# Kernel optimization log

Hardware: AMD Instinct MI355X
Metric: run time of the kernel (lower is better)

The kernel has to match this reference:

```python
import jax, jax.numpy as jnp
import numpy as np

EPS = 1.1920929e-07  # torch RMSNorm default eps = float32 finfo eps

def rms_norm(x, w):
    return x * jax.lax.rsqrt(jnp.mean(x * x, axis=-1, keepdims=True) + EPS) * w

def setup_inputs() -> dict:
    key = jax.random.key(0)
    ks = jax.random.split(key, 10)
    B, C, H, W = 8, 64, 48, 48
    E = C  # embed_dim = query_dim = key_dim = value_dim
    q = jax.random.normal(ks[0], (B, C, H, W), jnp.float32)
    k = jax.random.normal(ks[1], (B, C, H, W), jnp.float32)
    v = jax.random.normal(ks[2], (B, C, H, W), jnp.float32)
    s = 1.0 / np.sqrt(E)
    conv_w = jax.random.normal(ks[3], (C, C, 3, 3), jnp.float32) * (1.0 / np.sqrt(C * 9))
    nq_w = jnp.ones((E,), jnp.float32)
    nk_w = jnp.ones((E,), jnp.float32)
    wq = jax.random.normal(ks[4], (E, E), jnp.float32) * s
    bq = jax.random.normal(ks[5], (E,), jnp.float32) * 0.01
    wk = jax.random.normal(ks[6], (E, E), jnp.float32) * s
    bk = jax.random.normal(ks[7], (E,), jnp.float32) * 0.01
    return {"q": q, "k": k, "v": v, "conv_w": conv_w, "nq_w": nq_w,
            "nk_w": nk_w, "wq": wq, "bq": bq, "wk": wk, "bk": bk}

def reference(q, k, v, conv_w, nq_w, nk_w, wq, bq, wk, bk):
    B, C, H, W = q.shape
    num_heads = 4
    head_dim = C // num_heads
    # conv2d 3x3, stride 1, same padding, no bias
    qc = jax.lax.conv_general_dilated(
        q, conv_w, window_strides=(1, 1), padding='SAME',
        dimension_numbers=('NCHW', 'OIHW', 'NCHW'))
    # b c h w -> b (h w) c
    qs = qc.reshape(B, C, H * W).transpose(0, 2, 1)
    ksq = k.reshape(B, C, -1).transpose(0, 2, 1)
    vsq = v.reshape(B, C, -1).transpose(0, 2, 1)
    # RMSNorm on q and k (norm_v output feeds MHA value path whose output is discarded)
    qn = rms_norm(qs, nq_w)
    kn = rms_norm(ksq, nk_w)
    # MHA projections (q scaled by 1/sqrt(head_dim) as in torch)
    qp = (qn @ wq.T + bq) * (1.0 / np.sqrt(head_dim))
    kp = ksq_p = kn @ wk.T + bk
    Sq, Sk = qp.shape[1], kp.shape[1]
    qh = qp.reshape(B, Sq, num_heads, head_dim)
    kh = kp.reshape(B, Sk, num_heads, head_dim)
    scores = jnp.einsum('bihd,bjhd->bhij', qh, kh)
    attn = jax.nn.softmax(scores, axis=-1)
    # average_attn_weights=True -> mean over heads
    attn_avg = jnp.mean(attn, axis=1)  # [b, i, j]
    # custom output: weighted sum over RAW (un-normed, unprojected) value
    out = jnp.einsum('bij,bjd->bid', attn_avg, vsq)
    return out
```

## Files before the change

### kernel.cpp

```cpp
#include <hip/hip_runtime.h>
#include <hip/hip_bf16.h>

namespace {
constexpr int kB = 8;
constexpr int kC = 64;
constexpr int kH = 48;
constexpr int kW = 48;
constexpr int kS = kH * kW;
constexpr float kEps = 1.1920929e-07f;
constexpr float kQScale = 0.25f * 1.4426950408889634f;
}

typedef __attribute__((ext_vector_type(8))) short short8;
typedef __attribute__((ext_vector_type(4))) float f32x4;

__device__ __forceinline__ short f2bf(float x) {
  unsigned u = __float_as_uint(x);
  u += 0x7fffu + ((u >> 16) & 1u);
  return (short)(u >> 16);
}
__device__ __forceinline__ float bf2f(short s) {
  return __uint_as_float(((unsigned)(unsigned short)s) << 16);
}
__device__ __forceinline__ float fexp2(float x) {
  return __builtin_amdgcn_exp2f(x);
}

__global__ __launch_bounds__(256) void fused_prep(
    const float* __restrict__ q, const float* __restrict__ k,
    const float* __restrict__ v, const float* __restrict__ wq,
    const float* __restrict__ wk, const float* __restrict__ conv_w,
    short* __restrict__ qt, short* __restrict__ kt, short* __restrict__ vt,
    short* __restrict__ wqb3, short* __restrict__ wkb3, short* __restrict__ wt3) {
  const int blk = blockIdx.x;
  if (blk < 576) {
    __shared__ float tile[64][65];
    const int zz = blk / 36;
    const int bx = blk % 36;
    const int b = zz >> 1;
    const float* src = (zz & 1) ? k : q;
    short* dst = (zz & 1) ? kt : qt;
    const int s0 = bx * 64;
    const int tx = threadIdx.x & 63;
    const int ty = threadIdx.x >> 6;
#pragma unroll
    for (int r = 0; r < 16; ++r) {
      int c = r * 4 + ty;
      tile[c][tx] = src[((size_t)b * kC + c) * kS + s0 + tx];
    }
    __syncthreads();
#pragma unroll
    for (int r = 0; r < 16; ++r) {
      int s = r * 4 + ty;
      dst[((size_t)b * kS + s0 + s) * kC + tx] = f2bf(tile[tx][s]);
    }
  } else if (blk < 1728) {
    int idx = ((blk - 576) * 256 + threadIdx.x) * 4;
    float4 x = *reinterpret_cast<const float4*>(v + idx);
    int2 o;
    o.x = ((int)(unsigned short)f2bf(x.y) << 16) | (unsigned short)f2bf(x.x);
    o.y = ((int)(unsigned short)f2bf(x.w) << 16) | (unsigned short)f2bf(x.z);
    *reinterpret_cast<int2*>(vt + idx) = o;
  } else {
    int idx = (blk - 1728) * 256 + threadIdx.x;
    if (idx < 4096) {
      int j = idx & 7, Lw = (idx >> 3) & 63, slab = idx >> 9;
      int nt = slab & 3, kh = slab >> 2;
      int e = nt * 16 + (Lw & 15), c = kh * 32 + (Lw >> 4) * 8 + j;
      wqb3[idx] = f2bf(wq[e * 64 + c]);
    } else if (idx < 8192) {
      int i2 = idx - 4096;
      int j = i2 & 7, Lw = (i2 >> 3) & 63, slab = i2 >> 9;
      int nt = slab & 3, kh = slab >> 2;
      int e = nt * 16 + (Lw & 15), c = kh * 32 + (Lw >> 4) * 8 + j;
      wkb3[i2] = f2bf(wk[e * 64 + c]);
    } else {
      int i3 = idx - 8192;
      int j = i3 & 7, Lw = (i3 >> 3) & 63, slab = i3 >> 9;
      int nt = slab & 3, kh = (slab >> 2) & 1, tap = slab >> 3;
      int co = nt * 16 + (Lw & 15), ci = kh * 32 + (Lw >> 4) * 8 + j;
      wt3[i3] = f2bf(conv_w[co * 576 + ci * 9 + tap]);
    }
  }
}

__global__ __launch_bounds__(256) void fused_qk_gemm(
    const short* __restrict__ qt, const short* __restrict__ kt,
    const short* __restrict__ wt3, const short* __restrict__ wqb3,
    const short* __restrict__ wkb3,
    const float* __restrict__ nq_w, const float* __restrict__ nk_w,
    const float* __restrict__ bq, const float* __restrict__ bk,
    short* __restrict__ qp, short* __restrict__ kp) {
  __shared__ __align__(16) short Qs[164][72];
  __shared__ __align__(16) short ln[4][16][80];
  const int blk = blockIdx.x;
  const int t = threadIdx.x;
  const int ws = t >> 6;
  const int L = t & 63;
  const int quad = L >> 4;
  const int l16 = L & 15;
  const short8 zero8 = {0, 0, 0, 0, 0, 0, 0, 0};

  if (blk < 288) {
    const int b = blk / 36;
    const int S0 = (blk % 36) * 64;
    const int sBase = S0 + ws * 16;
    const int s = sBase + l16;
    const int h = s / kW, w = s % kW;

    const short* qtb = qt + (size_t)b * kS * kC;
#pragma unroll
    for (int it = 0; it < 6; ++it) {
      int idx = it * 256 + t;
      if (idx < 164 * 8) {
        int r = idx >> 3, sg = idx & 7;
        int srow = S0 - 49 + r;
        srow = srow < 0 ? 0 : (srow >= kS ? kS - 1 : srow);
        *reinterpret_cast<int4*>(&Qs[r][sg * 8]) =
            *reinterpret_cast<const int4*>(qtb + (size_t)srow * kC + sg * 8);
      }
    }
    __syncthreads();

    const int baseLocal = ws * 16 + l16 + 49;
    f32x4 acc[4] = {{0.f, 0.f, 0.f, 0.f}, {0.f, 0.f, 0.f, 0.f},
                    {0.f, 0.f, 0.f, 0.f}, {0.f, 0.f, 0.f, 0.f}};
#pragma unroll
    for (int tap = 0; tap < 9; ++tap) {
      const int dh = tap / 3 - 1, dw = tap % 3 - 1;
      const bool valid = (unsigned)(h + dh) < (unsigned)kH &&
                         (unsigned)(w + dw) < (unsigned)kW;
      const int local = baseLocal + dh * kW + dw;
#pragma unroll
      for (int kh = 0; kh < 2; ++kh) {
        short8 af = *reinterpret_cast<const short8*>(&Qs[local][kh * 32 + quad * 8]);
        af = valid ? af : zero8;
        const short* wb = wt3 + ((tap * 2 + kh) * 4) * 512 + L * 8;
#pragma unroll
        for (int nt = 0; nt < 4; ++nt) {
          short8 bf = *reinterpret_cast<const short8*>(wb + nt * 512);
          acc[nt] = __builtin_amdgcn_mfma_f32_16x16x32_bf16(af, bf, acc[nt], 0, 0, 0);
        }
      }
    }
    float rstd[4];
#pragma unroll
    for (int reg = 0; reg < 4; ++reg) {
      float pr = acc[0][reg] * acc[0][reg] + acc[1][reg] * acc[1][reg]
               + acc[2][reg] * acc[2][reg] + acc[3][reg] * acc[3][reg];
      pr += __shfl_xor(pr, 1, 64);
      pr += __shfl_xor(pr, 2, 64);
      pr += __shfl_xor(pr, 4, 64);
      pr += __shfl_xor(pr, 8, 64);
      rstd[reg] = rsqrtf(pr * (1.0f / kC) + kEps);
    }
#pragma unroll
    for (int nt = 0; nt < 4; ++nt) {
      float g = nq_w[nt * 16 + l16];
#pragma unroll
      for (int reg = 0; reg < 4; ++reg) {
        ln[ws][quad * 4 + reg][nt * 16 + l16] = f2bf(acc[nt][reg] * rstd[reg] * g);
      }
    }
    __syncthreads();
    f32x4 acc2[4] = {{0.f, 0.f, 0.f, 0.f}, {0.f, 0.f, 0.f, 0.f},
                     {0.f, 0.f, 0.f, 0.f}, {0.f, 0.f, 0.f, 0.f}};
#pragma unroll
    for (int kh = 0; kh < 2; ++kh) {
      short8 af = *reinterpret_cast<const short8*>(&ln[ws][l16][kh * 32 + quad * 8]);
      const short* wb = wqb3 + (kh * 4) * 512 + L * 8;
#pragma unroll
      for (int nt = 0; nt < 4; ++nt) {
        short8 bf = *reinterpret_cast<const short8*>(wb + nt * 512);
        acc2[nt] = __builtin_amdgcn_mfma_f32_16x16x32_bf16(af, bf, acc2[nt], 0, 0, 0);
      }
    }
#pragma unroll
    for (int nt = 0; nt < 4; ++nt) {
      const int e = nt * 16 + l16;
      float bias = bq[e];
#pragma unroll
      for (int reg = 0; reg < 4; ++reg) {
        qp[((size_t)b * kS + sBase + quad * 4 + reg) * kC + e] =
            f2bf((acc2[nt][reg] + bias) * kQScale);
      }
    }
  } else {
    const int idx = blk - 288;
    const int b = idx / 36;
    const int S0 = (idx % 36) * 64;
    const int sBase = S0 + ws * 16;

    const short* ktb = kt + ((size_t)b * kS + S0) * kC;
#pragma unroll
    for (int it = 0; it < 2; ++it) {
      int r = it * 32 + (t >> 3), sg = t & 7;
      *reinterpret_cast<int4*>(&Qs[r][sg * 8]) =
          *reinterpret_cast<const int4*>(ktb + (size_t)r * kC + sg * 8);
    }
    __syncthreads();

    short8 af0 = *reinterpret_cast<const short8*>(&Qs[ws * 16 + l16][quad * 8]);
    short8 af1 = *reinterpret_cast<const short8*>(&Qs[ws * 16 + l16][32 + quad * 8]);

    float xs[16];
#pragma unroll
    for (int j = 0; j < 8; ++j) { xs[j] = bf2f(af0[j]); xs[8 + j] = bf2f(af1[j]); }
    float sum = 0.f;
#pragma unroll
    for (int j = 0; j < 16; ++j) sum = fmaf(xs[j], xs[j], sum);
    sum += __shfl_xor(sum, 16, 64);
    sum += __shfl_xor(sum, 32, 64);
    float rstd = rsqrtf(sum * (1.0f / kC) + kEps);

    const float* n0 = nk_w + quad * 8;
#pragma unroll
    for (int j = 0; j < 8; ++j) {
      af0[j] = f2bf(xs[j] * rstd * n0[j]);
      af1[j] = f2bf(xs[8 + j] * rstd * n0[32 + j]);
    }

    f32x4 acc[4] = {{0.f, 0.f, 0.f, 0.f}, {0.f, 0.f, 0.f, 0.f},
                    {0.f, 0.f, 0.f, 0.f}, {0.f, 0.f, 0.f, 0.f}};
#pragma unroll
    for (int nt = 0; nt < 4; ++nt) {
      short8 bf0 = *reinterpret_cast<const short8*>(
          wkb3 + (0 * 4 + nt) * 512 + L * 8);
      short8 bf1 = *reinterpret_cast<const short8*>(
          wkb3 + (1 * 4 + nt) * 512 + L * 8);
      acc[nt] = __builtin_amdgcn_mfma_f32_16x16x32_bf16(af0, bf0, acc[nt], 0, 0, 0);
      acc[nt] = __builtin_amdgcn_mfma_f32_16x16x32_bf16(af1, bf1, acc[nt], 0, 0, 0);
    }
#pragma unroll
    for (int nt = 0; nt < 4; ++nt) {
      const int e = nt * 16 + l16;
      float bias = bk[e];
#pragma unroll
      for (int reg = 0; reg < 4; ++reg) {
        kp[((size_t)b * kS + sBase + quad * 4 + reg) * kC + e] =
            f2bf(acc[nt][reg] + bias);
      }
    }
  }
}

__global__ __launch_bounds__(256, 5) void attn_flash(
    const short* __restrict__ qp, const short* __restrict__ kp,
    const short* __restrict__ vt, float* __restrict__ out) {
  __shared__ __align__(16) short Kt[2][64][40];
  __shared__ __align__(16) short Vt[2][64][72];
  __shared__ float pl[4][16][2];
  __shared__ float Li[32][2];

  float* slabF = reinterpret_cast<float*>(&Kt[0][0][0]);

  const int blk = blockIdx.x;
  const int b = blk & 7;
  const int idx = blk >> 3;
  const int hp = idx & 1;
  const int i0 = (idx >> 1) * 32;
  const int t = threadIdx.x;
  const int ws = t >> 6;
  const int isub = ws & 1;
  const int jhalf = ws >> 1;
  const int jbase = jhalf * 32;
  const int L = t & 63;
  const int quad = L >> 4;
  const int l16 = L & 15;

  const f32x4 zc = {0.f, 0.f, 0.f, 0.f};
  const short8 z8 = {0, 0, 0, 0, 0, 0, 0, 0};

  const short* qrow = qp + ((size_t)b * kS + i0 + isub * 16 + l16) * kC + hp * 32;
  const short8 qw = *reinterpret_cast<const short8*>(qrow + quad * 8);
  const bool lo = quad < 2;
  const short8 qm[2] = {lo ? qw : z8, lo ? z8 : qw};

  const int rK = t >> 2;
  const int segK = t & 3;
  const int r8i = t >> 3;
  const int seg = t & 7;
  const short* kg = kp + (size_t)b * kS * kC + hp * 32;
  const short* vg = vt + (size_t)b * kC * kS;

  const int p32 = rK & 31;
  const int prowK =
      (rK & 32) | ((p32 & 4) << 2) | (((p32 >> 3) & 3) << 2) | (p32 & 3);

  int4 kreg, vreg[2];
  kreg = *reinterpret_cast<const int4*>(kg + (size_t)rK * kC + segK * 8);
#pragma unroll
  for (int pass = 0; pass < 2; ++pass)
    vreg[pass] = *reinterpret_cast<const int4*>(
        vg + (size_t)(pass * 32 + r8i) * kS + seg * 8);
  *reinterpret_cast<int4*>(&Kt[0][prowK][segK * 8]) = kreg;
#pragma unroll
  for (int pass = 0; pass < 2; ++pass)
    *reinterpret_cast<int4*>(&Vt[0][pass * 32 + r8i][seg * 8]) = vreg[pass];
  __syncthreads();

  f32x4 U[2][4];
#pragma unroll
  for (int hl = 0; hl < 2; ++hl)
#pragma unroll
    for (int d = 0; d < 4; ++d) U[hl][d] = zc;
  float lh[2] = {0.f, 0.f};

  for (int jt = 0; jt < kS / 64; ++jt) {
    const int buf = jt & 1;
    const bool more = (jt + 1) < kS / 64;
    if (more) {
      const int jn = (jt + 1) * 64;
      kreg = *reinterpret_cast<const int4*>(
          kg + (size_t)(jn + rK) * kC + segK * 8);
#pragma unroll
      for (int pass = 0; pass < 2; ++pass)
        vreg[pass] = *reinterpret_cast<const int4*>(
            vg + (size_t)(pass * 32 + r8i) * kS + jn + seg * 8);
    }

    short8 kf[2];
#pragma unroll
    for (int c = 0; c < 2; ++c)
      kf[c] = *reinterpret_cast<const short8*>(
          &Kt[buf][jbase + c * 16 + l16][quad * 8]);
    short8 vf[4];
#pragma unroll
    for (int d = 0; d < 4; ++d)
      vf[d] = *reinterpret_cast<const short8*>(
          &Vt[buf][d * 16 + l16][jbase + quad * 8]);

#pragma unroll
    for (int hl = 0; hl < 2; ++hl) {
      f32x4 s0 = __builtin_amdgcn_mfma_f32_16x16x32_bf16(kf[0], qm[hl], zc, 0, 0, 0);
      f32x4 s1 = __builtin_amdgcn_mfma_f32_16x16x32_bf16(kf[1], qm[hl], zc, 0, 0, 0);
      float e0 = fexp2(s0[0]), e1 = fexp2(s0[1]);
      float e2 = fexp2(s0[2]), e3 = fexp2(s0[3]);
      float f0 = fexp2(s1[0]), f1 = fexp2(s1[1]);
      float f2 = fexp2(s1[2]), f3 = fexp2(s1[3]);
      lh[hl] += ((e0 + e1) + (e2 + e3)) + ((f0 + f1) + (f2 + f3));
      union { __hip_bfloat162 h2[4]; short8 s8; } cv;
      cv.h2[0] = __float22bfloat162_rn(make_float2(e0, e1));
      cv.h2[1] = __float22bfloat162_rn(make_float2(e2, e3));
      cv.h2[2] = __float22bfloat162_rn(make_float2(f0, f1));
      cv.h2[3] = __float22bfloat162_rn(make_float2(f2, f3));
#pragma unroll
      for (int d = 0; d < 4; ++d)
        U[hl][d] = __builtin_amdgcn_mfma_f32_16x16x32_bf16(vf[d], cv.s8, U[hl][d], 0, 0, 0);
    }

    if (more) {
      const int nb = buf ^ 1;
      *reinterpret_cast<int4*>(&Kt[nb][prowK][segK * 8]) = kreg;
#pragma unroll
      for (int pass = 0; pass < 2; ++pass)
        *reinterpret_cast<int4*>(&Vt[nb][pass * 32 + r8i][seg * 8]) = vreg[pass];
    }
    __syncthreads();
  }

#pragma unroll
  for (int hl = 0; hl < 2; ++hl) {
    lh[hl] += __shfl_xor(lh[hl], 16, 64);
    lh[hl] += __shfl_xor(lh[hl], 32, 64);
  }
  if (quad == 0) {
#pragma unroll
    for (int hl = 0; hl < 2; ++hl) pl[ws][l16][hl] = lh[hl];
  }
  __syncthreads();
  if (t < 64) {
    const int i = t >> 1, h2 = t & 1;
    Li[i][h2] = 0.25f / (pl[i >> 4][i & 15][h2] + pl[(i >> 4) + 2][i & 15][h2]);
  }
  __syncthreads();
  float c2[2];
#pragma unroll
  for (int hl = 0; hl < 2; ++hl) c2[hl] = Li[isub * 16 + l16][hl];

#pragma unroll
  for (int d = 0; d < 4; ++d) {
    if (jhalf == 1) {
#pragma unroll
      for (int hl = 0; hl < 2; ++hl)
#pragma unroll
        for (int reg = 0; reg < 4; ++reg)
          slabF[((isub * 2 + hl) * 4 + reg) * 66 + L] = U[hl][d][reg];
    }
    __syncthreads();
    if (jhalf == 0) {
      float of[4] = {0.f, 0.f, 0.f, 0.f};
#pragma unroll
      for (int hl = 0; hl < 2; ++hl) {
#pragma unroll
        for (int reg = 0; reg < 4; ++reg) {
          float tot = U[hl][d][reg] + slabF[((isub * 2 + hl) * 4 + reg) * 66 + L];
          of[reg] += tot * c2[hl];
        }
      }
      float* op = out + ((size_t)b * kS + i0 + isub * 16 + l16) * kC + d * 16 + quad * 4;
#pragma unroll
      for (int reg = 0; reg < 4; ++reg) atomicAdd(op + reg, of[reg]);
    }
    __syncthreads();
  }
}

extern "C" void kernel_launch(void* const* d_in, const int* in_sizes, int n_in,
                              void* d_out, int out_size, void* d_ws, size_t ws_size,
                              hipStream_t stream) {
  const float* q      = (const float*)d_in[0];
  const float* k      = (const float*)d_in[1];
  const float* v      = (const float*)d_in[2];
  const float* conv_w = (const float*)d_in[3];
  const float* nq_w   = (const float*)d_in[4];
  const float* nk_w   = (const float*)d_in[5];
  const float* wq     = (const float*)d_in[6];
  const float* bq     = (const float*)d_in[7];
  const float* wk     = (const float*)d_in[8];
  const float* bk     = (const float*)d_in[9];
  float* out = (float*)d_out;

  const size_t N = (size_t)kB * kS * kC;
  short* qt   = (short*)d_ws;
  short* kt   = qt + N;
  short* vt   = kt + N;
  short* qp   = vt + N;
  short* kp   = qp + N;
  short* wqb3 = kp + N;
  short* wkb3 = wqb3 + 4096;
  short* wt3  = wkb3 + 4096;

  hipMemsetAsync(d_out, 0, out_size, stream);

  fused_prep<<<1904, 256, 0, stream>>>(q, k, v, wq, wk, conv_w,
                                       qt, kt, vt, wqb3, wkb3, wt3);
  fused_qk_gemm<<<576, 256, 0, stream>>>(qt, kt, wt3, wqb3, wkb3,
                                         nq_w, nk_w, bq, bk, qp, kp);
  attn_flash<<<1152, 256, 0, stream>>>(qp, kp, vt, out);
}
```

Measured before the change: 155.4 us.

## Load K/V fragments directly from global into registers, dropping LDS staging

```diff
diff --git a/kernel.cpp b/kernel.cpp
--- a/kernel.cpp
+++ b/kernel.cpp
@@ -244,15 +244,12 @@
   }
 }
 
-__global__ __launch_bounds__(256, 5) void attn_flash(
+__global__ __launch_bounds__(256, 4) void attn_flash(
     const short* __restrict__ qp, const short* __restrict__ kp,
     const short* __restrict__ vt, float* __restrict__ out) {
-  __shared__ __align__(16) short Kt[2][64][40];
-  __shared__ __align__(16) short Vt[2][64][72];
   __shared__ float pl[4][16][2];
   __shared__ float Li[32][2];
-
-  float* slabF = reinterpret_cast<float*>(&Kt[0][0][0]);
+  __shared__ __align__(16) float slab[16][66];
 
   const int blk = blockIdx.x;
   const int b = blk & 7;
@@ -263,7 +260,6 @@
   const int ws = t >> 6;
   const int isub = ws & 1;
   const int jhalf = ws >> 1;
-  const int jbase = jhalf * 32;
   const int L = t & 63;
   const int quad = L >> 4;
   const int l16 = L & 15;
@@ -276,28 +272,10 @@
   const bool lo = quad < 2;
   const short8 qm[2] = {lo ? qw : z8, lo ? z8 : qw};
 
-  const int rK = t >> 2;
-  const int segK = t & 3;
-  const int r8i = t >> 3;
-  const int seg = t & 7;
-  const short* kg = kp + (size_t)b * kS * kC + hp * 32;
-  const short* vg = vt + (size_t)b * kC * kS;
-
-  const int p32 = rK & 31;
-  const int prowK =
-      (rK & 32) | ((p32 & 4) << 2) | (((p32 >> 3) & 3) << 2) | (p32 & 3);
-
-  int4 kreg, vreg[2];
-  kreg = *reinterpret_cast<const int4*>(kg + (size_t)rK * kC + segK * 8);
-#pragma unroll
-  for (int pass = 0; pass < 2; ++pass)
-    vreg[pass] = *reinterpret_cast<const int4*>(
-        vg + (size_t)(pass * 32 + r8i) * kS + seg * 8);
-  *reinterpret_cast<int4*>(&Kt[0][prowK][segK * 8]) = kreg;
-#pragma unroll
-  for (int pass = 0; pass < 2; ++pass)
-    *reinterpret_cast<int4*>(&Vt[0][pass * 32 + r8i][seg * 8]) = vreg[pass];
-  __syncthreads();
+  const int permRow = ((l16 >> 2) << 3) | (l16 & 3);
+  const short* kbase =
+      kp + ((size_t)b * kS + jhalf * 32 + permRow) * kC + hp * 32 + quad * 8;
+  const short* vbase = vt + ((size_t)b * kC + l16) * kS + jhalf * 32 + quad * 8;
 
   f32x4 U[2][4];
 #pragma unroll
@@ -306,34 +284,33 @@
     for (int d = 0; d < 4; ++d) U[hl][d] = zc;
   float lh[2] = {0.f, 0.f};
 
+  short8 kn[2], vn[4];
+#pragma unroll
+  for (int c = 0; c < 2; ++c)
+    kn[c] = *reinterpret_cast<const short8*>(kbase + (size_t)c * 4 * kC);
+#pragma unroll
+  for (int d = 0; d < 4; ++d)
+    vn[d] = *reinterpret_cast<const short8*>(vbase + (size_t)d * 16 * kS);
+
   for (int jt = 0; jt < kS / 64; ++jt) {
-    const int buf = jt & 1;
-    const bool more = (jt + 1) < kS / 64;
-    if (more) {
-      const int jn = (jt + 1) * 64;
-      kreg = *reinterpret_cast<const int4*>(
-          kg + (size_t)(jn + rK) * kC + segK * 8);
-#pragma unroll
-      for (int pass = 0; pass < 2; ++pass)
-        vreg[pass] = *reinterpret_cast<const int4*>(
-            vg + (size_t)(pass * 32 + r8i) * kS + jn + seg * 8);
-    }
-
-    short8 kf[2];
-#pragma unroll
-    for (int c = 0; c < 2; ++c)
-      kf[c] = *reinterpret_cast<const short8*>(
-          &Kt[buf][jbase + c * 16 + l16][quad * 8]);
-    short8 vf[4];
-#pragma unroll
-    for (int d = 0; d < 4; ++d)
-      vf[d] = *reinterpret_cast<const short8*>(
-          &Vt[buf][d * 16 + l16][jbase + quad * 8]);
+    const short8 kf0 = kn[0], kf1 = kn[1];
+    const short8 vf0 = vn[0], vf1 = vn[1], vf2 = vn[2], vf3 = vn[3];
+
+    if (jt + 1 < kS / 64) {
+      const short* kb2 = kbase + (size_t)(jt + 1) * 64 * kC;
+      const short* vb2 = vbase + (size_t)(jt + 1) * 64;
+#pragma unroll
+      for (int c = 0; c < 2; ++c)
+        kn[c] = *reinterpret_cast<const short8*>(kb2 + (size_t)c * 4 * kC);
+#pragma unroll
+      for (int d = 0; d < 4; ++d)
+        vn[d] = *reinterpret_cast<const short8*>(vb2 + (size_t)d * 16 * kS);
+    }
 
 #pragma unroll
     for (int hl = 0; hl < 2; ++hl) {
-      f32x4 s0 = __builtin_amdgcn_mfma_f32_16x16x32_bf16(kf[0], qm[hl], zc, 0, 0, 0);
-      f32x4 s1 = __builtin_amdgcn_mfma_f32_16x16x32_bf16(kf[1], qm[hl], zc, 0, 0, 0);
+      f32x4 s0 = __builtin_amdgcn_mfma_f32_16x16x32_bf16(kf0, qm[hl], zc, 0, 0, 0);
+      f32x4 s1 = __builtin_amdgcn_mfma_f32_16x16x32_bf16(kf1, qm[hl], zc, 0, 0, 0);
       float e0 = fexp2(s0[0]), e1 = fexp2(s0[1]);
       float e2 = fexp2(s0[2]), e3 = fexp2(s0[3]);
       float f0 = fexp2(s1[0]), f1 = fexp2(s1[1]);
@@ -344,19 +321,11 @@
       cv.h2[1] = __float22bfloat162_rn(make_float2(e2, e3));
       cv.h2[2] = __float22bfloat162_rn(make_float2(f0, f1));
       cv.h2[3] = __float22bfloat162_rn(make_float2(f2, f3));
-#pragma unroll
-      for (int d = 0; d < 4; ++d)
-        U[hl][d] = __builtin_amdgcn_mfma_f32_16x16x32_bf16(vf[d], cv.s8, U[hl][d], 0, 0, 0);
-    }
-
-    if (more) {
-      const int nb = buf ^ 1;
-      *reinterpret_cast<int4*>(&Kt[nb][prowK][segK * 8]) = kreg;
-#pragma unroll
-      for (int pass = 0; pass < 2; ++pass)
-        *reinterpret_cast<int4*>(&Vt[nb][pass * 32 + r8i][seg * 8]) = vreg[pass];
-    }
-    __syncthreads();
+      U[hl][0] = __builtin_amdgcn_mfma_f32_16x16x32_bf16(vf0, cv.s8, U[hl][0], 0, 0, 0);
+      U[hl][1] = __builtin_amdgcn_mfma_f32_16x16x32_bf16(vf1, cv.s8, U[hl][1], 0, 0, 0);
+      U[hl][2] = __builtin_amdgcn_mfma_f32_16x16x32_bf16(vf2, cv.s8, U[hl][2], 0, 0, 0);
+      U[hl][3] = __builtin_amdgcn_mfma_f32_16x16x32_bf16(vf3, cv.s8, U[hl][3], 0, 0, 0);
+    }
   }
 
 #pragma unroll
@@ -385,7 +354,7 @@
       for (int hl = 0; hl < 2; ++hl)
 #pragma unroll
         for (int reg = 0; reg < 4; ++reg)
-          slabF[((isub * 2 + hl) * 4 + reg) * 66 + L] = U[hl][d][reg];
+          slab[(isub * 2 + hl) * 4 + reg][L] = U[hl][d][reg];
     }
     __syncthreads();
     if (jhalf == 0) {
@@ -394,7 +363,7 @@
       for (int hl = 0; hl < 2; ++hl) {
 #pragma unroll
         for (int reg = 0; reg < 4; ++reg) {
-          float tot = U[hl][d][reg] + slabF[((isub * 2 + hl) * 4 + reg) * 66 + L];
+          float tot = U[hl][d][reg] + slab[(isub * 2 + hl) * 4 + reg][L];
           of[reg] += tot * c2[hl];
         }
       }
```

After: 236.6 us. 52.3% more time.
